# Kernel optimization log

Hardware: AMD Instinct MI355X
Metric: run time of the kernel (lower is better)

Reference implementation:

```python
import jax, jax.numpy as jnp
import numpy as np

B, H, W, C = 4, 512, 512, 32
PAD = 3          # padding init arg
SHIFT = 0.0      # threshold(0.5) - 0.5


def setup_inputs() -> dict:
    key = jax.random.key(0)
    x = jax.random.normal(key, (B, H, W, C), dtype=jnp.float32)
    return {"inputs": x}


def _detect_rect(x):
    # x: [B,H,W,C] -> per-(b,c) bbox via thresholded row/col max scans
    i32 = jnp.int32
    x_scan = jnp.round(jax.nn.sigmoid(jnp.max(x, axis=1)) + SHIFT).astype(i32)  # [B,W,C] in {0,1}
    y_scan = jnp.round(jax.nn.sigmoid(jnp.max(x, axis=2)) + SHIFT).astype(i32)  # [B,H,C]
    wx = jnp.arange(W, dtype=i32)
    wy = jnp.arange(H, dtype=i32)
    # decreasing weights -> argmax picks first active index (min); increasing -> last active (max)
    x_min = jnp.argmax(x_scan * wx[::-1][None, :, None], axis=1).astype(i32)  # [B,C]
    x_max = jnp.argmax(x_scan * wx[None, :, None], axis=1).astype(i32)
    y_min = jnp.argmax(y_scan * wy[::-1][None, :, None], axis=1).astype(i32)
    y_max = jnp.argmax(y_scan * wy[None, :, None], axis=1).astype(i32)
    return x_min, y_min, x_max, y_max


def _focus_one(img, xm, ym, xM, yM):
    # img: [H,W]. Crop [ym:yM, xm:xM], bilinear resize (TF1 legacy, preserve aspect
    # ratio to fit max(H-2p, hc) x max(W-2p, wc)), then center crop-or-pad to (H,W).
    f32, i32 = jnp.float32, jnp.int32
    hc = jnp.maximum(yM - ym, 1)
    wc = jnp.maximum(xM - xm, 1)
    zh = jnp.maximum(H - 2 * PAD, hc)
    zw = jnp.maximum(W - 2 * PAD, wc)
    scale = jnp.minimum(zh.astype(f32) / hc.astype(f32), zw.astype(f32) / wc.astype(f32))
    rh = jnp.round(scale * hc.astype(f32)).astype(i32)  # resized height
    rw = jnp.round(scale * wc.astype(f32)).astype(i32)  # resized width
    oi = jnp.arange(H, dtype=i32)[:, None]
    oj = jnp.arange(W, dtype=i32)[None, :]
    # crop_or_pad: pad_top=(H-rh)//2 if rh<H else crop_top=(rh-H)//2
    ri = oi - jnp.maximum(0, (H - rh) // 2) + jnp.maximum(0, (rh - H) // 2)
    rj = oj - jnp.maximum(0, (W - rw) // 2) + jnp.maximum(0, (rw - W) // 2)
    valid = (ri >= 0) & (ri < rh) & (rj >= 0) & (rj < rw)
    # TF1 legacy bilinear (align_corners=False, no half-pixel): src = dst * in/out
    sy = ri.astype(f32) * (hc.astype(f32) / rh.astype(f32))
    sx = rj.astype(f32) * (wc.astype(f32) / rw.astype(f32))
    y0 = jnp.clip(jnp.floor(sy).astype(i32), 0, hc - 1)
    x0 = jnp.clip(jnp.floor(sx).astype(i32), 0, wc - 1)
    y1 = jnp.minimum(y0 + 1, hc - 1)
    x1 = jnp.minimum(x0 + 1, wc - 1)
    wy_ = jnp.clip(sy - y0.astype(f32), 0.0, 1.0)
    wx_ = jnp.clip(sx - x0.astype(f32), 0.0, 1.0)
    Y0 = jnp.clip(ym + y0, 0, H - 1)
    Y1 = jnp.clip(ym + y1, 0, H - 1)
    X0 = jnp.clip(xm + x0, 0, W - 1)
    X1 = jnp.clip(xm + x1, 0, W - 1)
    v00 = img[Y0, X0]
    v01 = img[Y0, X1]
    v10 = img[Y1, X0]
    v11 = img[Y1, X1]
    top = v00 * (1.0 - wx_) + v01 * wx_
    bot = v10 * (1.0 - wx_) + v11 * wx_
    out = top * (1.0 - wy_) + bot * wy_
    return jnp.where(valid, out, 0.0)


def reference(inputs):
    x_min, y_min, x_max, y_max = _detect_rect(inputs)  # each [B,C]
    imgs = jnp.transpose(inputs, (0, 3, 1, 2)).reshape(B * C, H, W)
    out = jax.vmap(_focus_one)(
        imgs, x_min.reshape(-1), y_min.reshape(-1), x_max.reshape(-1), y_max.reshape(-1)
    )  # [B*C, H, W]
    return jnp.transpose(out.reshape(B, C, H, W), (0, 2, 3, 1))
```

## Files before the change

### kernel.cpp

```cpp
#include <hip/hip_runtime.h>
#include <math.h>

#define BB 4
#define HH 512
#define WW 512
#define CC 32
#define PADC 3
#define NHK 16
#define NWK 16

typedef float f4nat __attribute__((ext_vector_type(4)));

struct Params {
    int ym, xm, hc, wc, rh, rw, dy, dx;
    float ry, rx;
};

struct FastRec {
    int flag, iLo, iHi, jLo, jHi, dY, dX, pad;
};

__device__ __forceinline__ unsigned int pos_bit(float v) { return v > 0.0f ? 1u : 0u; }

__global__ __launch_bounds__(256) void scan_kernel(const float* __restrict__ x,
                                                   unsigned int* __restrict__ rowpart,
                                                   unsigned int* __restrict__ colpart,
                                                   float* __restrict__ out) {
    const int blk = blockIdx.x;
    const int b = blk >> 8;
    const int hk = (blk >> 4) & 15;
    const int wk = blk & 15;
    const int t = threadIdx.x;
    const int c4 = t & 7;
    const int wi = t >> 3;

    __shared__ unsigned int rowbuf[32][4];

    size_t f0 = ((size_t)(b * HH + hk * 32) * WW + wk * 32 + wi) * (CC / 4) + c4;
    const f4nat* xin = (const f4nat*)x;
    f4nat* xout = (f4nat*)out;

    unsigned int colacc = 0;
    #pragma unroll 4
    for (int r = 0; r < 32; ++r) {
        size_t idx = f0 + (size_t)r * (WW * CC / 4);
        f4nat v = xin[idx];
        __builtin_nontemporal_store(v, xout + idx);
        unsigned int nib = pos_bit(v.x) | (pos_bit(v.y) << 1) |
                           (pos_bit(v.z) << 2) | (pos_bit(v.w) << 3);
        unsigned int m = nib << (c4 * 4);
        m |= __shfl_xor(m, 1);
        m |= __shfl_xor(m, 2);
        m |= __shfl_xor(m, 4);
        colacc |= m;
        unsigned int rm = m;
        rm |= __shfl_xor(rm, 8);
        rm |= __shfl_xor(rm, 16);
        rm |= __shfl_xor(rm, 32);
        if ((t & 63) == 0) rowbuf[r][t >> 6] = rm;
    }
    if (c4 == 0)
        colpart[(size_t)(hk * BB + b) * WW + wk * 32 + wi] = colacc;
    __syncthreads();
    if (t < 32) {
        unsigned int rw = rowbuf[t][0] | rowbuf[t][1] | rowbuf[t][2] | rowbuf[t][3];
        rowpart[(size_t)(wk * BB + b) * HH + hk * 32 + t] = rw;
    }
}

__global__ __launch_bounds__(1024) void bboxfin_kernel(const unsigned int* __restrict__ rowpart,
                                                       const unsigned int* __restrict__ colpart,
                                                       Params* __restrict__ prm,
                                                       FastRec* __restrict__ fast) {
    const int b = blockIdx.x;
    const int t = threadIdx.x;
    __shared__ unsigned int colmask[WW];
    __shared__ unsigned int rowmask[HH];
    if (t < WW) {
        unsigned int a = 0;
        #pragma unroll
        for (int k = 0; k < NHK; ++k) a |= colpart[(size_t)(k * BB + b) * WW + t];
        colmask[t] = a;
    } else {
        const int h = t - WW;
        unsigned int a = 0;
        #pragma unroll
        for (int k = 0; k < NWK; ++k) a |= rowpart[(size_t)(k * BB + b) * HH + h];
        rowmask[h] = a;
    }
    __syncthreads();
    const int c = t >> 5, lane = t & 31;
    int fx = WW, lx = -1, fy = HH, ly = -1;
    for (int m = 0; m < WW / 32; ++m) {
        int w = m * 32 + lane;
        if ((colmask[w] >> c) & 1u) { fx = min(fx, w); lx = max(lx, w); }
        if ((rowmask[w] >> c) & 1u) { fy = min(fy, w); ly = max(ly, w); }
    }
    for (int off = 16; off; off >>= 1) {
        fx = min(fx, __shfl_xor(fx, off));
        lx = max(lx, __shfl_xor(lx, off));
        fy = min(fy, __shfl_xor(fy, off));
        ly = max(ly, __shfl_xor(ly, off));
    }
    __shared__ Params sp[CC];
    __shared__ int ok[CC];
    if (lane == 0) {
        int xm = (fx <= WW - 2) ? fx : 0;
        int xM = (lx >= 0) ? lx : 0;
        int ym = (fy <= HH - 2) ? fy : 0;
        int yM = (ly >= 0) ? ly : 0;
        int hc = max(yM - ym, 1), wc = max(xM - xm, 1);
        int zh = max(HH - 2 * PADC, hc), zw = max(WW - 2 * PADC, wc);
        float scale = fminf((float)zh / (float)hc, (float)zw / (float)wc);
        int rh = (int)rintf(scale * (float)hc);
        int rw = (int)rintf(scale * (float)wc);
        int pad_y = max(0, (HH - rh) / 2), crop_y = max(0, (rh - HH) / 2);
        int pad_x = max(0, (WW - rw) / 2), crop_x = max(0, (rw - WW) / 2);
        Params p;
        p.ym = ym; p.xm = xm; p.hc = hc; p.wc = wc; p.rh = rh; p.rw = rw;
        p.dy = pad_y - crop_y; p.dx = pad_x - crop_x;
        p.ry = (float)hc / (float)rh;
        p.rx = (float)wc / (float)rw;
        sp[c] = p;
    }
    __syncthreads();
    if (t < CC) {
        Params p = sp[t];
        const Params& p0 = sp[0];
        bool simple = (p.rh == p.hc) && (p.rw == p.wc);
        bool same = (p.ym == p0.ym) && (p.xm == p0.xm) && (p.dy == p0.dy) &&
                    (p.dx == p0.dx) && (p.rh == p0.rh) && (p.rw == p0.rw);
        ok[t] = (simple && same) ? 1 : 0;
        prm[b * CC + t] = p;
    }
    __syncthreads();
    if (t == 0) {
        int all = 1;
        for (int k = 0; k < CC; ++k) all &= ok[k];
        Params p0 = sp[0];
        FastRec f;
        f.flag = all;
        f.iLo = p0.dy; f.iHi = p0.dy + p0.rh;
        f.jLo = p0.dx; f.jHi = p0.dx + p0.rw;
        f.dY = p0.ym - p0.dy; f.dX = p0.xm - p0.dx;
        f.pad = 0;
        fast[b] = f;
    }
}

__global__ __launch_bounds__(256) void fixup_kernel(const float* __restrict__ x,
                                                    const Params* __restrict__ prm,
                                                    const FastRec* __restrict__ fast,
                                                    float* __restrict__ out) {
    const int blk = blockIdx.x;
    const int t = threadIdx.x;
    const int b = blk >> 8, loc = blk & 255;
    FastRec f = fast[b];
    bool ident = f.flag && f.dY == 0 && f.dX == 0 && f.iLo == 0 && f.jLo == 0;
    if (ident) {
        if (loc >= 32) return;
        const int rowsZ = HH - f.iHi;
        const int W8 = (WW - f.jHi) * 8;
        const int rowElems = rowsZ * (WW * CC / 4);
        const int total = rowElems + f.iHi * W8;
        for (int u = loc * 256 + t; u < total; u += 8192) {
            size_t q;
            if (u < rowElems) {
                int i = f.iHi + (u >> 12);
                int r = u & 4095;
                q = ((size_t)b << 21) | ((size_t)i << 12) | r;
            } else {
                int v = u - rowElems;
                int i = v / W8;
                int r = v - i * W8;
                int j = f.jHi + (r >> 3);
                q = ((size_t)b << 21) | ((size_t)i << 12) | ((size_t)j << 3) | (r & 7);
            }
            __builtin_nontemporal_store((f4nat)0.0f, (f4nat*)out + q);
        }
        return;
    }
    __shared__ Params sp[CC];
    {
        const int nw = CC * (int)(sizeof(Params) / 4);
        const int* src = (const int*)(prm + b * CC);
        int* dst = (int*)sp;
        for (int k = t; k < nw; k += 256) dst[k] = src[k];
    }
    __syncthreads();
    const float* base = x + (size_t)b * ((size_t)HH * WW * CC);
    for (int u = loc * 256 + t; u < HH * WW * CC / 4; u += 65536) {
        const int c0 = (u & 7) * 4;
        const int j = (u >> 3) & 511;
        const int i = u >> 12;
        f4nat r;
        #pragma unroll
        for (int k = 0; k < 4; ++k) {
            Params p = sp[c0 + k];
            int ri = i - p.dy, rj = j - p.dx;
            bool valid = (ri >= 0) && (ri < p.rh) && (rj >= 0) && (rj < p.rw);
            float sy = (float)ri * p.ry;
            float sx = (float)rj * p.rx;
            int y0 = min(max((int)floorf(sy), 0), p.hc - 1);
            int x0 = min(max((int)floorf(sx), 0), p.wc - 1);
            int y1 = min(y0 + 1, p.hc - 1);
            int x1 = min(x0 + 1, p.wc - 1);
            float wy = fminf(fmaxf(sy - (float)y0, 0.0f), 1.0f);
            float wx = fminf(fmaxf(sx - (float)x0, 0.0f), 1.0f);
            int Y0 = min(p.ym + y0, HH - 1);
            int Y1 = min(p.ym + y1, HH - 1);
            int X0 = min(p.xm + x0, WW - 1);
            int X1 = min(p.xm + x1, WW - 1);
            float v00 = base[((size_t)Y0 * WW + X0) * CC + c0 + k];
            float v01 = base[((size_t)Y0 * WW + X1) * CC + c0 + k];
            float v10 = base[((size_t)Y1 * WW + X0) * CC + c0 + k];
            float v11 = base[((size_t)Y1 * WW + X1) * CC + c0 + k];
            float top = v00 * (1.0f - wx) + v01 * wx;
            float bot = v10 * (1.0f - wx) + v11 * wx;
            float o = top * (1.0f - wy) + bot * wy;
            r[k] = valid ? o : 0.0f;
        }
        __builtin_nontemporal_store(r, (f4nat*)out + (((size_t)b << 21) + u));
    }
}

extern "C" void kernel_launch(void* const* d_in, const int* in_sizes, int n_in,
                              void* d_out, int out_size, void* d_ws, size_t ws_size,
                              hipStream_t stream) {
    const float* x = (const float*)d_in[0];
    float* out = (float*)d_out;
    unsigned char* ws = (unsigned char*)d_ws;
    unsigned int* colpart = (unsigned int*)ws;
    unsigned int* rowpart = (unsigned int*)(ws + 131072);
    Params* prm = (Params*)(ws + 262144);
    FastRec* fast = (FastRec*)(ws + 267264);

    hipLaunchKernelGGL(scan_kernel, dim3(BB * NHK * NWK), dim3(256), 0, stream,
                       x, rowpart, colpart, out);
    hipLaunchKernelGGL(bboxfin_kernel, dim3(BB), dim3(1024), 0, stream,
                       rowpart, colpart, prm, fast);
    hipLaunchKernelGGL(fixup_kernel, dim3(1024), dim3(256), 0, stream,
                       x, prm, fast, out);
}
```

Measured before the change: 55.47 us.

## Fuse bbox finalization into fixup kernel and use nontemporal loads in scan

Merges the single-block-per-batch bbox finalization kernel into the fixup kernel. Each of the 1024 fixup blocks now redundantly rebuilds the row/column masks and the per-channel params in shared memory, which removes one kernel launch and the workspace round trip for the params. Each thread group handles 4 channels so the work fits in 256 threads. The scan kernel also switches its input loads to nontemporal. The cost is redundant mask reduction and bbox math in every block, reading about 64KB of partial masks per block.

After: 70.74 us. 27.5% more time.

```diff
diff --git a/kernel.cpp b/kernel.cpp
--- a/kernel.cpp
+++ b/kernel.cpp
@@ -44,7 +44,7 @@
     #pragma unroll 4
     for (int r = 0; r < 32; ++r) {
         size_t idx = f0 + (size_t)r * (WW * CC / 4);
-        f4nat v = xin[idx];
+        f4nat v = __builtin_nontemporal_load(xin + idx);
         __builtin_nontemporal_store(v, xout + idx);
         unsigned int nib = pos_bit(v.x) | (pos_bit(v.y) << 1) |
                            (pos_bit(v.z) << 2) | (pos_bit(v.w) << 3);
@@ -68,60 +68,67 @@
     }
 }
 
-__global__ __launch_bounds__(1024) void bboxfin_kernel(const unsigned int* __restrict__ rowpart,
-                                                       const unsigned int* __restrict__ colpart,
-                                                       Params* __restrict__ prm,
-                                                       FastRec* __restrict__ fast) {
-    const int b = blockIdx.x;
+__global__ __launch_bounds__(256) void fixfin_kernel(const float* __restrict__ x,
+                                                     const unsigned int* __restrict__ rowpart,
+                                                     const unsigned int* __restrict__ colpart,
+                                                     float* __restrict__ out) {
+    const int blk = blockIdx.x;
+    const int b = blk >> 8, loc = blk & 255;
     const int t = threadIdx.x;
     __shared__ unsigned int colmask[WW];
     __shared__ unsigned int rowmask[HH];
-    if (t < WW) {
+    for (int u = t; u < WW; u += 256) {
         unsigned int a = 0;
         #pragma unroll
-        for (int k = 0; k < NHK; ++k) a |= colpart[(size_t)(k * BB + b) * WW + t];
-        colmask[t] = a;
-    } else {
-        const int h = t - WW;
+        for (int k = 0; k < NHK; ++k) a |= colpart[(size_t)(k * BB + b) * WW + u];
+        colmask[u] = a;
+    }
+    for (int u = t; u < HH; u += 256) {
         unsigned int a = 0;
         #pragma unroll
-        for (int k = 0; k < NWK; ++k) a |= rowpart[(size_t)(k * BB + b) * HH + h];
-        rowmask[h] = a;
-    }
-    __syncthreads();
-    const int c = t >> 5, lane = t & 31;
-    int fx = WW, lx = -1, fy = HH, ly = -1;
-    for (int m = 0; m < WW / 32; ++m) {
-        int w = m * 32 + lane;
-        if ((colmask[w] >> c) & 1u) { fx = min(fx, w); lx = max(lx, w); }
-        if ((rowmask[w] >> c) & 1u) { fy = min(fy, w); ly = max(ly, w); }
-    }
-    for (int off = 16; off; off >>= 1) {
-        fx = min(fx, __shfl_xor(fx, off));
-        lx = max(lx, __shfl_xor(lx, off));
-        fy = min(fy, __shfl_xor(fy, off));
-        ly = max(ly, __shfl_xor(ly, off));
-    }
+        for (int k = 0; k < NWK; ++k) a |= rowpart[(size_t)(k * BB + b) * HH + u];
+        rowmask[u] = a;
+    }
+    __syncthreads();
+
     __shared__ Params sp[CC];
     __shared__ int ok[CC];
-    if (lane == 0) {
-        int xm = (fx <= WW - 2) ? fx : 0;
-        int xM = (lx >= 0) ? lx : 0;
-        int ym = (fy <= HH - 2) ? fy : 0;
-        int yM = (ly >= 0) ? ly : 0;
-        int hc = max(yM - ym, 1), wc = max(xM - xm, 1);
-        int zh = max(HH - 2 * PADC, hc), zw = max(WW - 2 * PADC, wc);
-        float scale = fminf((float)zh / (float)hc, (float)zw / (float)wc);
-        int rh = (int)rintf(scale * (float)hc);
-        int rw = (int)rintf(scale * (float)wc);
-        int pad_y = max(0, (HH - rh) / 2), crop_y = max(0, (rh - HH) / 2);
-        int pad_x = max(0, (WW - rw) / 2), crop_x = max(0, (rw - WW) / 2);
-        Params p;
-        p.ym = ym; p.xm = xm; p.hc = hc; p.wc = wc; p.rh = rh; p.rw = rw;
-        p.dy = pad_y - crop_y; p.dx = pad_x - crop_x;
-        p.ry = (float)hc / (float)rh;
-        p.rx = (float)wc / (float)rw;
-        sp[c] = p;
+    __shared__ FastRec sf;
+    const int g = t >> 5, lane = t & 31;
+    #pragma unroll
+    for (int q = 0; q < 4; ++q) {
+        const int c = g * 4 + q;
+        int fx = WW, lx = -1, fy = HH, ly = -1;
+        for (int m = 0; m < WW / 32; ++m) {
+            int w = m * 32 + lane;
+            if ((colmask[w] >> c) & 1u) { fx = min(fx, w); lx = max(lx, w); }
+            if ((rowmask[w] >> c) & 1u) { fy = min(fy, w); ly = max(ly, w); }
+        }
+        for (int off = 16; off; off >>= 1) {
+            fx = min(fx, __shfl_xor(fx, off));
+            lx = max(lx, __shfl_xor(lx, off));
+            fy = min(fy, __shfl_xor(fy, off));
+            ly = max(ly, __shfl_xor(ly, off));
+        }
+        if (lane == 0) {
+            int xm = (fx <= WW - 2) ? fx : 0;
+            int xM = (lx >= 0) ? lx : 0;
+            int ym = (fy <= HH - 2) ? fy : 0;
+            int yM = (ly >= 0) ? ly : 0;
+            int hc = max(yM - ym, 1), wc = max(xM - xm, 1);
+            int zh = max(HH - 2 * PADC, hc), zw = max(WW - 2 * PADC, wc);
+            float scale = fminf((float)zh / (float)hc, (float)zw / (float)wc);
+            int rh = (int)rintf(scale * (float)hc);
+            int rw = (int)rintf(scale * (float)wc);
+            int pad_y = max(0, (HH - rh) / 2), crop_y = max(0, (rh - HH) / 2);
+            int pad_x = max(0, (WW - rw) / 2), crop_x = max(0, (rw - WW) / 2);
+            Params p;
+            p.ym = ym; p.xm = xm; p.hc = hc; p.wc = wc; p.rh = rh; p.rw = rw;
+            p.dy = pad_y - crop_y; p.dx = pad_x - crop_x;
+            p.ry = (float)hc / (float)rh;
+            p.rx = (float)wc / (float)rw;
+            sp[c] = p;
+        }
     }
     __syncthreads();
     if (t < CC) {
@@ -131,7 +138,6 @@
         bool same = (p.ym == p0.ym) && (p.xm == p0.xm) && (p.dy == p0.dy) &&
                     (p.dx == p0.dx) && (p.rh == p0.rh) && (p.rw == p0.rw);
         ok[t] = (simple && same) ? 1 : 0;
-        prm[b * CC + t] = p;
     }
     __syncthreads();
     if (t == 0) {
@@ -144,18 +150,11 @@
         f.jLo = p0.dx; f.jHi = p0.dx + p0.rw;
         f.dY = p0.ym - p0.dy; f.dX = p0.xm - p0.dx;
         f.pad = 0;
-        fast[b] = f;
-    }
-}
-
-__global__ __launch_bounds__(256) void fixup_kernel(const float* __restrict__ x,
-                                                    const Params* __restrict__ prm,
-                                                    const FastRec* __restrict__ fast,
-                                                    float* __restrict__ out) {
-    const int blk = blockIdx.x;
-    const int t = threadIdx.x;
-    const int b = blk >> 8, loc = blk & 255;
-    FastRec f = fast[b];
+        sf = f;
+    }
+    __syncthreads();
+    FastRec f = sf;
+
     bool ident = f.flag && f.dY == 0 && f.dX == 0 && f.iLo == 0 && f.jLo == 0;
     if (ident) {
         if (loc >= 32) return;
@@ -180,14 +179,6 @@
         }
         return;
     }
-    __shared__ Params sp[CC];
-    {
-        const int nw = CC * (int)(sizeof(Params) / 4);
-        const int* src = (const int*)(prm + b * CC);
-        int* dst = (int*)sp;
-        for (int k = t; k < nw; k += 256) dst[k] = src[k];
-    }
-    __syncthreads();
     const float* base = x + (size_t)b * ((size_t)HH * WW * CC);
     for (int u = loc * 256 + t; u < HH * WW * CC / 4; u += 65536) {
         const int c0 = (u & 7) * 4;
@@ -232,13 +223,9 @@
     unsigned char* ws = (unsigned char*)d_ws;
     unsigned int* colpart = (unsigned int*)ws;
     unsigned int* rowpart = (unsigned int*)(ws + 131072);
-    Params* prm = (Params*)(ws + 262144);
-    FastRec* fast = (FastRec*)(ws + 267264);
 
     hipLaunchKernelGGL(scan_kernel, dim3(BB * NHK * NWK), dim3(256), 0, stream,
                        x, rowpart, colpart, out);
-    hipLaunchKernelGGL(bboxfin_kernel, dim3(BB), dim3(1024), 0, stream,
-                       rowpart, colpart, prm, fast);
-    hipLaunchKernelGGL(fixup_kernel, dim3(1024), dim3(256), 0, stream,
-                       x, prm, fast, out);
+    hipLaunchKernelGGL(fixfin_kernel, dim3(BB * 256), dim3(256), 0, stream,
+                       x, rowpart, colpart, out);
 }
```
